# Optimization experiments

Measured on AMD Instinct MI355X. Metric: run time of the kernel, lower is better.

The kernel has to match this reference:

```python
import jax, jax.numpy as jnp
import numpy as np

EXPERT_NUM = 16
TOP_K = 2
BALANCE_WT = 0.01
EPS = 1e-9


def setup_inputs() -> dict:
    key = jax.random.key(0)
    ks = jax.random.split(key, 4)
    B, D, E, O = 8192, 4096, EXPERT_NUM, 512
    features = jax.random.normal(ks[0], (B, D), dtype=jnp.float32)
    W_r = jax.random.normal(ks[1], (D, E), dtype=jnp.float32) * (1.0 / np.sqrt(D))
    b_r = jnp.zeros((E,), dtype=jnp.float32)
    W_e = jax.random.normal(ks[2], (E, D, O), dtype=jnp.float32) * (1.0 / np.sqrt(D))
    b_e = jnp.zeros((E, O), dtype=jnp.float32)
    return {"features": features, "W_r": W_r, "b_r": b_r, "W_e": W_e, "b_e": b_e}


def reference(features, W_r, b_r, W_e, b_e):
    # Router: softmax over experts. [B, E]
    routing_prob = jax.nn.softmax(features @ W_r + b_r, axis=-1)
    # Top-k selection and renormalized combine weights. [B, K]
    top_values, top_indices = jax.lax.top_k(routing_prob, TOP_K)
    weights = top_values / jnp.clip(top_values.sum(axis=1, keepdims=True), EPS)
    # Dense all-expert compute (as the original does). [B, E, O]
    expert_outputs = jnp.einsum('bd,edo->beo', features, W_e) + b_e
    # Gather top-k expert outputs. [B, K, O]
    gathered = jnp.take_along_axis(expert_outputs, top_indices[:, :, None], axis=1)
    logits = jnp.sum(weights[:, :, None] * gathered, axis=1)  # [B, O]
    # Load-balance loss: KL(pi || uniform) scaled by balance_wt.
    pi = routing_prob.mean(axis=0)
    balance_loss = BALANCE_WT * (
        jnp.sum(pi * jnp.log(jnp.clip(pi, EPS)))
        + jnp.log(jnp.asarray(EXPERT_NUM, dtype=pi.dtype))
    )
    return logits, balance_loss
```

## Files before the change

### kernel.cpp

```cpp
#include <hip/hip_runtime.h>


#define B_ 8192
#define D_ 4096
#define E_ 16
#define O_ 512

typedef unsigned int uint32;
typedef unsigned short ushort_t;
typedef __bf16 bf16_t;
typedef bf16_t bf16x8 __attribute__((ext_vector_type(8)));
typedef float f32x4 __attribute__((ext_vector_type(4)));
typedef ushort_t u16x8 __attribute__((ext_vector_type(8)));

__device__ __forceinline__ uint32 bf16_rne(float x) {
  uint32 u = __float_as_uint(x);
  return (u + 0x7fffu + ((u >> 16) & 1u)) >> 16;
}
__device__ __forceinline__ float bf16_to_f32(ushort_t u) {
  return __uint_as_float(((uint32)u) << 16);
}
__device__ __forceinline__ f32x4 ntload4(const float* p) {
  return __builtin_nontemporal_load((const f32x4*)p);
}

__device__ __forceinline__ void gload16(const void* g, void* l) {
  __builtin_amdgcn_global_load_lds(
      (const __attribute__((address_space(1))) void*)g,
      (__attribute__((address_space(3))) void*)l, 16, 0, 0);
}

__global__ __launch_bounds__(256) void wr_transpose(
    const float* __restrict__ Wr, float* __restrict__ WrT) {
  const int d = blockIdx.x * 256 + threadIdx.x;
  const float* src = &Wr[(size_t)d * 16];
  f32x4 v0 = ntload4(src), v1 = ntload4(src + 4);
  f32x4 v2 = ntload4(src + 8), v3 = ntload4(src + 12);
  WrT[0 * D_ + d] = v0[0];  WrT[1 * D_ + d] = v0[1];
  WrT[2 * D_ + d] = v0[2];  WrT[3 * D_ + d] = v0[3];
  WrT[4 * D_ + d] = v1[0];  WrT[5 * D_ + d] = v1[1];
  WrT[6 * D_ + d] = v1[2];  WrT[7 * D_ + d] = v1[3];
  WrT[8 * D_ + d] = v2[0];  WrT[9 * D_ + d] = v2[1];
  WrT[10 * D_ + d] = v2[2]; WrT[11 * D_ + d] = v2[3];
  WrT[12 * D_ + d] = v3[0]; WrT[13 * D_ + d] = v3[1];
  WrT[14 * D_ + d] = v3[2]; WrT[15 * D_ + d] = v3[3];
}

__global__ __launch_bounds__(256) void prep(
    const float* __restrict__ feat, const float* __restrict__ WrT,
    const float* __restrict__ br, const float* __restrict__ We,
    ushort_t* __restrict__ featbf, ushort_t* __restrict__ Wbt,
    int* __restrict__ idxP, float2* __restrict__ wP,
    float* __restrict__ pblk) {
  __shared__ __align__(16) float shmem[64 * 65];
  const int tid = threadIdx.x;

  if (blockIdx.x < 512) {
    const int lane = tid & 63, w = tid >> 6;
    const int tbase = blockIdx.x * 16 + w * 4;

    float acc[4][16] = {};

    for (int si = 0; si < 8; ++si) {
      const int d8 = si * 512 + lane * 8;
      f32x4 fa[4], fb[4];
#pragma unroll
      for (int i = 0; i < 4; ++i) {
        const float* fp = &feat[(size_t)(tbase + i) * D_ + d8];
        fa[i] = ntload4(fp);
        fb[i] = ntload4(fp + 4);
      }
#pragma unroll
      for (int i = 0; i < 4; ++i) {
        uint4 pk;
        pk.x = bf16_rne(fa[i][0]) | (bf16_rne(fa[i][1]) << 16);
        pk.y = bf16_rne(fa[i][2]) | (bf16_rne(fa[i][3]) << 16);
        pk.z = bf16_rne(fb[i][0]) | (bf16_rne(fb[i][1]) << 16);
        pk.w = bf16_rne(fb[i][2]) | (bf16_rne(fb[i][3]) << 16);
        *(uint4*)&featbf[(size_t)(tbase + i) * D_ + d8] = pk;
      }
#pragma unroll
      for (int e = 0; e < 16; ++e) {
        const float* wp = &WrT[(size_t)e * D_ + d8];
        f32x4 wa = *(const f32x4*)wp;
        f32x4 wb = *(const f32x4*)(wp + 4);
#pragma unroll
        for (int i = 0; i < 4; ++i) {
          float a = acc[i][e];
          a = fmaf(fa[i][0], wa[0], a);
          a = fmaf(fa[i][1], wa[1], a);
          a = fmaf(fa[i][2], wa[2], a);
          a = fmaf(fa[i][3], wa[3], a);
          a = fmaf(fb[i][0], wb[0], a);
          a = fmaf(fb[i][1], wb[1], a);
          a = fmaf(fb[i][2], wb[2], a);
          a = fmaf(fb[i][3], wb[3], a);
          acc[i][e] = a;
        }
      }
    }

    float psum[16];
#pragma unroll
    for (int e = 0; e < 16; ++e) psum[e] = 0.f;

#pragma unroll
    for (int i = 0; i < 4; ++i) {
      float l[16];
#pragma unroll
      for (int e = 0; e < 16; ++e) {
        float v = acc[i][e];
#pragma unroll
        for (int m = 32; m >= 1; m >>= 1) v += __shfl_xor(v, m, 64);
        l[e] = v + br[e];
      }
      float mx = l[0];
#pragma unroll
      for (int e = 1; e < 16; ++e) mx = fmaxf(mx, l[e]);
      float p[16];
      float s = 0.f;
#pragma unroll
      for (int e = 0; e < 16; ++e) { p[e] = expf(l[e] - mx); s += p[e]; }
      float inv = 1.f / s;
#pragma unroll
      for (int e = 0; e < 16; ++e) { p[e] *= inv; psum[e] += p[e]; }
      int i0 = 0; float v0 = p[0];
#pragma unroll
      for (int e = 1; e < 16; ++e) if (p[e] > v0) { v0 = p[e]; i0 = e; }
      int i1 = (i0 == 0) ? 1 : 0; float v1 = p[i1];
#pragma unroll
      for (int e = 0; e < 16; ++e)
        if (e != i0 && p[e] > v1) { v1 = p[e]; i1 = e; }
      float denom = fmaxf(v0 + v1, 1e-9f);
      if (lane == 0) {
        int t = tbase + i;
        idxP[t] = i0 | (i1 << 8);
        wP[t] = make_float2(v0 / denom, v1 / denom);
      }
    }
    if (lane == 0) {
#pragma unroll
      for (int e = 0; e < 16; ++e) shmem[w * 16 + e] = psum[e];
    }
    __syncthreads();
    if (tid < 16)
      pblk[blockIdx.x * 16 + tid] =
          (shmem[tid] + shmem[16 + tid]) + (shmem[32 + tid] + shmem[48 + tid]);
  } else {
    const int tx = tid & 15, ty = tid >> 4;
    const int wid = blockIdx.x - 512;
    f32x4 cur[4], nxt[4];
    {
      const int tix = wid * 4;
      const int e = tix >> 9;
      const int rem = tix & 511;
      const int d0 = (rem >> 3) << 6, o0 = (rem & 7) << 6;
      const float* src = We + ((size_t)e * D_ + d0) * O_ + o0;
#pragma unroll
      for (int p = 0; p < 4; ++p)
        cur[p] = ntload4(src + (size_t)(ty + p * 16) * O_ + tx * 4);
    }
#pragma unroll
    for (int q = 0; q < 4; ++q) {
      const int tix = wid * 4 + q;
      const int e = tix >> 9;
      const int rem = tix & 511;
      const int d0 = (rem >> 3) << 6, o0 = (rem & 7) << 6;
      if (q) __syncthreads();
#pragma unroll
      for (int p = 0; p < 4; ++p) {
        int dl = ty + p * 16;
        shmem[dl * 65 + tx * 4 + 0] = cur[p][0];
        shmem[dl * 65 + tx * 4 + 1] = cur[p][1];
        shmem[dl * 65 + tx * 4 + 2] = cur[p][2];
        shmem[dl * 65 + tx * 4 + 3] = cur[p][3];
      }
      if (q < 3) {
        const int tix2 = tix + 1;
        const int e2 = tix2 >> 9;
        const int rem2 = tix2 & 511;
        const int d02 = (rem2 >> 3) << 6, o02 = (rem2 & 7) << 6;
        const float* src2 = We + ((size_t)e2 * D_ + d02) * O_ + o02;
#pragma unroll
        for (int p = 0; p < 4; ++p)
          nxt[p] = ntload4(src2 + (size_t)(ty + p * 16) * O_ + tx * 4);
      }
      __syncthreads();
      ushort_t* dst = Wbt + ((size_t)e * O_ + o0) * D_ + d0;
#pragma unroll
      for (int p = 0; p < 4; ++p) {
        int ol = ty + p * 16;
        uint2 pk;
        pk.x = bf16_rne(shmem[(tx * 4 + 0) * 65 + ol]) |
               (bf16_rne(shmem[(tx * 4 + 1) * 65 + ol]) << 16);
        pk.y = bf16_rne(shmem[(tx * 4 + 2) * 65 + ol]) |
               (bf16_rne(shmem[(tx * 4 + 3) * 65 + ol]) << 16);
        *(uint2*)(dst + (size_t)ol * D_ + tx * 4) = pk;
      }
#pragma unroll
      for (int p = 0; p < 4; ++p) cur[p] = nxt[p];
    }
  }
}

__global__ __launch_bounds__(256) void bucket(
    const int* __restrict__ idxP, const float2* __restrict__ wP,
    int* __restrict__ tokL, float* __restrict__ wgtL, int* __restrict__ cntA,
    int* __restrict__ posA, int* __restrict__ posB) {
  const int e = blockIdx.x;
  const int tid = threadIdx.x, lane = tid & 63, w = tid >> 6;
  __shared__ int wsum[4];
  __shared__ int basev;
  if (tid == 0) basev = 0;
  __syncthreads();

  for (int c = 0; c < B_; c += 256) {
    const int t = c + tid;
    const int pk = idxP[t];
    const float2 wv = wP[t];
    const bool m0 = (pk & 255) == e;
    const bool m1 = (pk >> 8) == e;
    const bool m = m0 || m1;
    const float wt = m0 ? wv.x : wv.y;
    unsigned long long bal = __ballot(m);
    int rank = __popcll(bal & ((1ull << lane) - 1ull));
    if (lane == 0) wsum[w] = __popcll(bal);
    __syncthreads();
    int wbase = basev;
    for (int q = 0; q < w; ++q) wbase += wsum[q];
    if (m) {
      int pos = wbase + rank;
      tokL[e * B_ + pos] = t;
      wgtL[e * B_ + pos] = wt;
      if (m0) posA[t] = pos; else posB[t] = pos;
    }
    __syncthreads();
    if (tid == 0) basev += (wsum[0] + wsum[1]) + (wsum[2] + wsum[3]);
  }
  __syncthreads();
  if (tid == 0) cntA[e] = basev;
}

#define VM3 asm volatile("s_waitcnt vmcnt(3)" ::: "memory")
#define VM0 asm volatile("s_waitcnt vmcnt(0)" ::: "memory")

__global__ __launch_bounds__(512, 4) void moe_gemm(
    const ushort_t* __restrict__ featbf, const ushort_t* __restrict__ Wbt,
    const float* __restrict__ be, const int* __restrict__ tokL,
    const float* __restrict__ wgtL, const int* __restrict__ cntA,
    ushort_t* __restrict__ g0, ushort_t* __restrict__ g1,
    float* __restrict__ out, int dense) {
  const int orig = blockIdx.x;
  const int work = (orig & 7) * 512 + (orig >> 3);
  const int z = work >> 7;
  const int e = z >> 1, khalf = z & 1;
  const int cnt = cntA[e];
  const int row0 = ((work >> 1) & 63) * 128;
  if (row0 >= cnt) return;
  const int o0 = (work & 1) * 256;

  const int tid = threadIdx.x;
  const int lane = tid & 63, w = tid >> 6;
  const int wm = w >> 2, wn = w & 3;

  __shared__ __align__(16) ushort_t As[3][128 * 32];
  __shared__ __align__(16) ushort_t Bs[3][256 * 32];

  const int kg = (lane & 3) ^ ((lane >> 3) & 3);
  const size_t kbase = (size_t)khalf * 2048 + kg * 8;
  const int arow = row0 + w * 16 + (lane >> 2);
  const int atok = (arow < cnt) ? tokL[e * B_ + arow] : 0;
  const ushort_t* aS = featbf + (size_t)atok * D_ + kbase;
  const ushort_t* bS[2];
#pragma unroll
  for (int j = 0; j < 2; ++j) {
    int r = (2 * w + j) * 16 + (lane >> 2);
    bS[j] = Wbt + ((size_t)e * O_ + o0 + r) * D_ + kbase;
  }

  f32x4 acc[4][4] = {};
  const int lr = lane & 15;
  const int lg = lane >> 4;
  const int ps = (lg ^ ((lr >> 1) & 3)) * 8;

#define STAGE(buf, t)                                                \
  {                                                                  \
    gload16(aS + (t) * 32, &As[buf][(w * 16) * 32]);                 \
    gload16(bS[0] + (t) * 32, &Bs[buf][(2 * w) * 512]);              \
    gload16(bS[1] + (t) * 32, &Bs[buf][(2 * w + 1) * 512]);          \
  }

#define COMPUTE(buf)                                                 \
  {                                                                  \
    bf16x8 af[4], bf[4];                                             \
    _Pragma("unroll") for (int m = 0; m < 4; ++m)                    \
        af[m] = *(const bf16x8*)&As[buf][(wm * 64 + m * 16 + lr) * 32 + ps]; \
    _Pragma("unroll") for (int n = 0; n < 4; ++n)                    \
        bf[n] = *(const bf16x8*)&Bs[buf][(wn * 64 + n * 16 + lr) * 32 + ps]; \
    __builtin_amdgcn_s_setprio(1);                                   \
    _Pragma("unroll") for (int m = 0; m < 4; ++m)                    \
        _Pragma("unroll") for (int n = 0; n < 4; ++n)                \
            acc[m][n] = __builtin_amdgcn_mfma_f32_16x16x32_bf16(     \
                af[m], bf[n], acc[m][n], 0, 0, 0);                   \
    __builtin_amdgcn_s_setprio(0);                                   \
  }

  STAGE(0, 0);
  STAGE(1, 1);
  for (int tt = 0; tt < 20; ++tt) {
    const int t = tt * 3;
    VM3; __builtin_amdgcn_s_barrier(); COMPUTE(0); STAGE(2, t + 2);
    VM3; __builtin_amdgcn_s_barrier(); COMPUTE(1); STAGE(0, t + 3);
    VM3; __builtin_amdgcn_s_barrier(); COMPUTE(2); STAGE(1, t + 4);
  }
  VM3; __builtin_amdgcn_s_barrier(); COMPUTE(0); STAGE(2, 62);
  VM3; __builtin_amdgcn_s_barrier(); COMPUTE(1); STAGE(0, 63);
  VM3; __builtin_amdgcn_s_barrier(); COMPUTE(2);
  VM0; __builtin_amdgcn_s_barrier(); COMPUTE(0);

  if (dense) {
    int base = 0;
#pragma unroll
    for (int j = 0; j < 16; ++j) base += (j < e) ? cntA[j] : 0;
    ushort_t* G = khalf ? g1 : g0;
#pragma unroll
    for (int m = 0; m < 4; ++m) {
#pragma unroll
      for (int i = 0; i < 4; ++i) {
        int gr = row0 + wm * 64 + m * 16 + (lane >> 4) * 4 + i;
        if (gr < cnt) {
#pragma unroll
          for (int n = 0; n < 4; ++n) {
            int o = o0 + wn * 64 + n * 16 + (lane & 15);
            G[(size_t)(base + gr) * O_ + o] = (ushort_t)bf16_rne(acc[m][n][i]);
          }
        }
      }
    }
  } else {
#pragma unroll
    for (int m = 0; m < 4; ++m) {
#pragma unroll
      for (int i = 0; i < 4; ++i) {
        int gr = row0 + wm * 64 + m * 16 + (lane >> 4) * 4 + i;
        if (gr < cnt) {
          int tk = tokL[e * B_ + gr];
          float wt = wgtL[e * B_ + gr];
#pragma unroll
          for (int n = 0; n < 4; ++n) {
            int o = o0 + wn * 64 + n * 16 + (lane & 15);
            float v = acc[m][n][i] + (khalf ? 0.f : be[e * O_ + o]);
            atomicAdd(&out[(size_t)tk * O_ + o], wt * v);
          }
        }
      }
    }
  }
#undef STAGE
#undef COMPUTE
}

__global__ __launch_bounds__(256) void combine(
    const ushort_t* __restrict__ g0, const ushort_t* __restrict__ g1,
    const int* __restrict__ idxP, const float2* __restrict__ wP,
    const int* __restrict__ posA, const int* __restrict__ posB,
    const int* __restrict__ cntA, const float* __restrict__ be,
    const float* __restrict__ pblk, float* __restrict__ out) {
  const int tid = threadIdx.x;
  const int t = blockIdx.x * 4 + (tid >> 6);
  const int o = (tid & 63) * 8;
  const int pk = idxP[t];
  const int e0 = pk & 255, e1 = pk >> 8;
  const float2 wv = wP[t];
  int s = 0, off0 = 0, off1 = 0;
#pragma unroll
  for (int j = 0; j < 16; ++j) {
    if (j == e0) off0 = s;
    if (j == e1) off1 = s;
    s += cntA[j];
  }
  const size_t s0 = (size_t)(off0 + posA[t]) * O_ + o;
  const size_t s1 = (size_t)(off1 + posB[t]) * O_ + o;
  u16x8 a0 = *(const u16x8*)&g0[s0];
  u16x8 a1 = *(const u16x8*)&g1[s0];
  u16x8 b0 = *(const u16x8*)&g0[s1];
  u16x8 b1 = *(const u16x8*)&g1[s1];
  const float* be0 = &be[e0 * O_ + o];
  const float* be1 = &be[e1 * O_ + o];
  float r[8];
#pragma unroll
  for (int j = 0; j < 8; ++j) {
    float a = bf16_to_f32(a0[j]) + bf16_to_f32(a1[j]) + be0[j];
    float b = bf16_to_f32(b0[j]) + bf16_to_f32(b1[j]) + be1[j];
    r[j] = wv.x * a + wv.y * b;
  }
  *(f32x4*)&out[(size_t)t * O_ + o] = f32x4{r[0], r[1], r[2], r[3]};
  *(f32x4*)&out[(size_t)t * O_ + o + 4] = f32x4{r[4], r[5], r[6], r[7]};

  if (blockIdx.x == 0) {
    __shared__ float red[64];
    if (tid < 64) {
      const int e = tid & 15, g = tid >> 4;
      float acc = 0.f;
      for (int b = g; b < 512; b += 4) acc += pblk[b * 16 + e];
      red[tid] = acc;
    }
    __syncthreads();
    if (tid < 16) {
      float tot = (red[tid] + red[16 + tid]) + (red[32 + tid] + red[48 + tid]);
      float pi = tot * (1.f / (float)B_);
      red[tid] = pi * logf(fmaxf(pi, 1e-9f));
    }
    __syncthreads();
    if (tid == 0) {
      float loss = 0.f;
#pragma unroll
      for (int e2 = 0; e2 < 16; ++e2) loss += red[e2];
      out[(size_t)B_ * O_] = 0.01f * (loss + logf(16.f));
    }
  }
}

__global__ __launch_bounds__(64) void finalize(const float* __restrict__ pblk,
                                               float* __restrict__ out) {
  __shared__ float red[64];
  const int tid = threadIdx.x;
  const int e = tid & 15, g = tid >> 4;
  float s = 0.f;
  for (int b = g; b < 512; b += 4) s += pblk[b * 16 + e];
  red[tid] = s;
  __syncthreads();
  if (tid < 16) {
    float tot = (red[tid] + red[16 + tid]) + (red[32 + tid] + red[48 + tid]);
    float pi = tot * (1.f / (float)B_);
    red[tid] = pi * logf(fmaxf(pi, 1e-9f));
  }
  __syncthreads();
  if (tid == 0) {
    float loss = 0.f;
#pragma unroll
    for (int e2 = 0; e2 < 16; ++e2) loss += red[e2];
    out[(size_t)B_ * O_] = 0.01f * (loss + logf(16.f));
  }
}

extern "C" void kernel_launch(void* const* d_in, const int* in_sizes, int n_in,
                              void* d_out, int out_size, void* d_ws,
                              size_t ws_size, hipStream_t stream) {
  const float* feat = (const float*)d_in[0];
  const float* Wr = (const float*)d_in[1];
  const float* br = (const float*)d_in[2];
  const float* We = (const float*)d_in[3];
  const float* be = (const float*)d_in[4];
  float* out = (float*)d_out;

  char* ws = (char*)d_ws;
  const size_t SZG     = (size_t)(2 * B_) * O_ * 2;
  const size_t OFF_FEAT = 67108864;
  const size_t OFF_G0   = OFF_FEAT + 67108864;
  const size_t OFF_G1   = OFF_G0 + SZG;
  const size_t OFF_TOK  = OFF_G1 + SZG;
  const size_t OFF_WGT  = OFF_TOK + 524288;
  const size_t OFF_CNT  = OFF_WGT + 524288;
  const size_t OFF_IDX  = OFF_CNT + 256;
  const size_t OFF_WP   = OFF_IDX + 32768;
  const size_t OFF_PB   = OFF_WP + 65536;
  const size_t OFF_PA   = OFF_PB + 32768;
  const size_t OFF_PBo  = OFF_PA + 32768;
  const size_t OFF_WRT  = OFF_PBo + 32768;
  const size_t NEED     = OFF_WRT + 262144;
  ushort_t* Wbt = (ushort_t*)ws;
  ushort_t* featbf = (ushort_t*)(ws + OFF_FEAT);
  ushort_t* g0 = (ushort_t*)(ws + OFF_G0);
  ushort_t* g1 = (ushort_t*)(ws + OFF_G1);
  int* tokL = (int*)(ws + OFF_TOK);
  float* wgtL = (float*)(ws + OFF_WGT);
  int* cntA = (int*)(ws + OFF_CNT);
  int* idxP = (int*)(ws + OFF_IDX);
  float2* wP = (float2*)(ws + OFF_WP);
  float* pblk = (float*)(ws + OFF_PB);
  int* posA = (int*)(ws + OFF_PA);
  int* posB = (int*)(ws + OFF_PBo);
  float* WrT = (float*)(ws + OFF_WRT);
  const int dense = ws_size >= NEED ? 1 : 0;

  if (!dense)
    hipMemsetAsync(out, 0, (size_t)(B_ * O_ + 1) * sizeof(float), stream);

  wr_transpose<<<D_ / 256, 256, 0, stream>>>(Wr, WrT);
  prep<<<512 + 2048, 256, 0, stream>>>(feat, WrT, br, We, featbf, Wbt, idxP,
                                       wP, pblk);
  bucket<<<E_, 256, 0, stream>>>(idxP, wP, tokL, wgtL, cntA, posA, posB);
  moe_gemm<<<4096, 512, 0, stream>>>(featbf, Wbt, be, tokL, wgtL, cntA, g0,
                                     g1, out, dense);
  if (dense)
    combine<<<B_ / 4, 256, 0, stream>>>(g0, g1, idxP, wP, posA, posB, cntA,
                                        be, pblk, out);
  else
    finalize<<<1, 64, 0, stream>>>(pblk, out);
}
```

Measured before the change: 258.5 us.

## Scatter expert GEMM outputs to token-indexed rows and halve router tokens per block

The expert GEMM epilogue now writes each result row straight to a token-indexed slot (first or second choice, chosen through idxP), replacing the compacted per-expert layout. This removes the posA/posB bookkeeping in bucket, the prefix-sum over counts in both the GEMM and combine, and makes combine's reads contiguous by token. Separately, the router part of prep now handles 2 tokens per wave across 1024 blocks instead of 4 tokens across 512, giving more parallelism but loading the router weights more times. The scattered GEMM stores lose some locality, and each stored row needs an extra tokL/idxP lookup.

```diff
diff --git a/kernel.cpp b/kernel.cpp
--- a/kernel.cpp
+++ b/kernel.cpp
@@ -55,23 +55,23 @@
   __shared__ __align__(16) float shmem[64 * 65];
   const int tid = threadIdx.x;
 
-  if (blockIdx.x < 512) {
+  if (blockIdx.x < 1024) {
     const int lane = tid & 63, w = tid >> 6;
-    const int tbase = blockIdx.x * 16 + w * 4;
-
-    float acc[4][16] = {};
+    const int tbase = blockIdx.x * 8 + w * 2;
+
+    float acc[2][16] = {};
 
     for (int si = 0; si < 8; ++si) {
       const int d8 = si * 512 + lane * 8;
-      f32x4 fa[4], fb[4];
-#pragma unroll
-      for (int i = 0; i < 4; ++i) {
+      f32x4 fa[2], fb[2];
+#pragma unroll
+      for (int i = 0; i < 2; ++i) {
         const float* fp = &feat[(size_t)(tbase + i) * D_ + d8];
         fa[i] = ntload4(fp);
         fb[i] = ntload4(fp + 4);
       }
 #pragma unroll
-      for (int i = 0; i < 4; ++i) {
+      for (int i = 0; i < 2; ++i) {
         uint4 pk;
         pk.x = bf16_rne(fa[i][0]) | (bf16_rne(fa[i][1]) << 16);
         pk.y = bf16_rne(fa[i][2]) | (bf16_rne(fa[i][3]) << 16);
@@ -85,7 +85,7 @@
         f32x4 wa = *(const f32x4*)wp;
         f32x4 wb = *(const f32x4*)(wp + 4);
 #pragma unroll
-        for (int i = 0; i < 4; ++i) {
+        for (int i = 0; i < 2; ++i) {
           float a = acc[i][e];
           a = fmaf(fa[i][0], wa[0], a);
           a = fmaf(fa[i][1], wa[1], a);
@@ -105,7 +105,7 @@
     for (int e = 0; e < 16; ++e) psum[e] = 0.f;
 
 #pragma unroll
-    for (int i = 0; i < 4; ++i) {
+    for (int i = 0; i < 2; ++i) {
       float l[16];
 #pragma unroll
       for (int e = 0; e < 16; ++e) {
@@ -148,7 +148,7 @@
           (shmem[tid] + shmem[16 + tid]) + (shmem[32 + tid] + shmem[48 + tid]);
   } else {
     const int tx = tid & 15, ty = tid >> 4;
-    const int wid = blockIdx.x - 512;
+    const int wid = blockIdx.x - 1024;
     f32x4 cur[4], nxt[4];
     {
       const int tix = wid * 4;
@@ -205,8 +205,7 @@
 
 __global__ __launch_bounds__(256) void bucket(
     const int* __restrict__ idxP, const float2* __restrict__ wP,
-    int* __restrict__ tokL, float* __restrict__ wgtL, int* __restrict__ cntA,
-    int* __restrict__ posA, int* __restrict__ posB) {
+    int* __restrict__ tokL, float* __restrict__ wgtL, int* __restrict__ cntA) {
   const int e = blockIdx.x;
   const int tid = threadIdx.x, lane = tid & 63, w = tid >> 6;
   __shared__ int wsum[4];
@@ -232,7 +231,6 @@
       int pos = wbase + rank;
       tokL[e * B_ + pos] = t;
       wgtL[e * B_ + pos] = wt;
-      if (m0) posA[t] = pos; else posB[t] = pos;
     }
     __syncthreads();
     if (tid == 0) basev += (wsum[0] + wsum[1]) + (wsum[2] + wsum[3]);
@@ -248,8 +246,8 @@
     const ushort_t* __restrict__ featbf, const ushort_t* __restrict__ Wbt,
     const float* __restrict__ be, const int* __restrict__ tokL,
     const float* __restrict__ wgtL, const int* __restrict__ cntA,
-    ushort_t* __restrict__ g0, ushort_t* __restrict__ g1,
-    float* __restrict__ out, int dense) {
+    const int* __restrict__ idxP, ushort_t* __restrict__ g0,
+    ushort_t* __restrict__ g1, float* __restrict__ out, int dense) {
   const int orig = blockIdx.x;
   const int work = (orig & 7) * 512 + (orig >> 3);
   const int z = work >> 7;
@@ -319,9 +317,6 @@
   VM0; __builtin_amdgcn_s_barrier(); COMPUTE(0);
 
   if (dense) {
-    int base = 0;
-#pragma unroll
-    for (int j = 0; j < 16; ++j) base += (j < e) ? cntA[j] : 0;
     ushort_t* G = khalf ? g1 : g0;
 #pragma unroll
     for (int m = 0; m < 4; ++m) {
@@ -329,10 +324,12 @@
       for (int i = 0; i < 4; ++i) {
         int gr = row0 + wm * 64 + m * 16 + (lane >> 4) * 4 + i;
         if (gr < cnt) {
+          int tk = tokL[e * B_ + gr];
+          size_t row = ((idxP[tk] & 255) == e) ? (size_t)tk : (size_t)(B_ + tk);
 #pragma unroll
           for (int n = 0; n < 4; ++n) {
             int o = o0 + wn * 64 + n * 16 + (lane & 15);
-            G[(size_t)(base + gr) * O_ + o] = (ushort_t)bf16_rne(acc[m][n][i]);
+            G[row * O_ + o] = (ushort_t)bf16_rne(acc[m][n][i]);
           }
         }
       }
@@ -363,24 +360,16 @@
 __global__ __launch_bounds__(256) void combine(
     const ushort_t* __restrict__ g0, const ushort_t* __restrict__ g1,
     const int* __restrict__ idxP, const float2* __restrict__ wP,
-    const int* __restrict__ posA, const int* __restrict__ posB,
-    const int* __restrict__ cntA, const float* __restrict__ be,
-    const float* __restrict__ pblk, float* __restrict__ out) {
+    const float* __restrict__ be, const float* __restrict__ pblk,
+    float* __restrict__ out) {
   const int tid = threadIdx.x;
   const int t = blockIdx.x * 4 + (tid >> 6);
   const int o = (tid & 63) * 8;
   const int pk = idxP[t];
   const int e0 = pk & 255, e1 = pk >> 8;
   const float2 wv = wP[t];
-  int s = 0, off0 = 0, off1 = 0;
-#pragma unroll
-  for (int j = 0; j < 16; ++j) {
-    if (j == e0) off0 = s;
-    if (j == e1) off1 = s;
-    s += cntA[j];
-  }
-  const size_t s0 = (size_t)(off0 + posA[t]) * O_ + o;
-  const size_t s1 = (size_t)(off1 + posB[t]) * O_ + o;
+  const size_t s0 = (size_t)t * O_ + o;
+  const size_t s1 = (size_t)(B_ + t) * O_ + o;
   u16x8 a0 = *(const u16x8*)&g0[s0];
   u16x8 a1 = *(const u16x8*)&g1[s0];
   u16x8 b0 = *(const u16x8*)&g0[s1];
@@ -402,7 +391,7 @@
     if (tid < 64) {
       const int e = tid & 15, g = tid >> 4;
       float acc = 0.f;
-      for (int b = g; b < 512; b += 4) acc += pblk[b * 16 + e];
+      for (int b = g; b < 1024; b += 4) acc += pblk[b * 16 + e];
       red[tid] = acc;
     }
     __syncthreads();
@@ -427,7 +416,7 @@
   const int tid = threadIdx.x;
   const int e = tid & 15, g = tid >> 4;
   float s = 0.f;
-  for (int b = g; b < 512; b += 4) s += pblk[b * 16 + e];
+  for (int b = g; b < 1024; b += 4) s += pblk[b * 16 + e];
   red[tid] = s;
   __syncthreads();
   if (tid < 16) {
@@ -465,9 +454,7 @@
   const size_t OFF_IDX  = OFF_CNT + 256;
   const size_t OFF_WP   = OFF_IDX + 32768;
   const size_t OFF_PB   = OFF_WP + 65536;
-  const size_t OFF_PA   = OFF_PB + 32768;
-  const size_t OFF_PBo  = OFF_PA + 32768;
-  const size_t OFF_WRT  = OFF_PBo + 32768;
+  const size_t OFF_WRT  = OFF_PB + 65536;
   const size_t NEED     = OFF_WRT + 262144;
   ushort_t* Wbt = (ushort_t*)ws;
   ushort_t* featbf = (ushort_t*)(ws + OFF_FEAT);
@@ -479,8 +466,6 @@
   int* idxP = (int*)(ws + OFF_IDX);
   float2* wP = (float2*)(ws + OFF_WP);
   float* pblk = (float*)(ws + OFF_PB);
-  int* posA = (int*)(ws + OFF_PA);
-  int* posB = (int*)(ws + OFF_PBo);
   float* WrT = (float*)(ws + OFF_WRT);
   const int dense = ws_size >= NEED ? 1 : 0;
 
@@ -488,14 +473,13 @@
     hipMemsetAsync(out, 0, (size_t)(B_ * O_ + 1) * sizeof(float), stream);
 
   wr_transpose<<<D_ / 256, 256, 0, stream>>>(Wr, WrT);
-  prep<<<512 + 2048, 256, 0, stream>>>(feat, WrT, br, We, featbf, Wbt, idxP,
-                                       wP, pblk);
-  bucket<<<E_, 256, 0, stream>>>(idxP, wP, tokL, wgtL, cntA, posA, posB);
-  moe_gemm<<<4096, 512, 0, stream>>>(featbf, Wbt, be, tokL, wgtL, cntA, g0,
-                                     g1, out, dense);
+  prep<<<1024 + 2048, 256, 0, stream>>>(feat, WrT, br, We, featbf, Wbt, idxP,
+                                        wP, pblk);
+  bucket<<<E_, 256, 0, stream>>>(idxP, wP, tokL, wgtL, cntA);
+  moe_gemm<<<4096, 512, 0, stream>>>(featbf, Wbt, be, tokL, wgtL, cntA, idxP,
+                                     g0, g1, out, dense);
   if (dense)
-    combine<<<B_ / 4, 256, 0, stream>>>(g0, g1, idxP, wP, posA, posB, cntA,
-                                        be, pblk, out);
+    combine<<<B_ / 4, 256, 0, stream>>>(g0, g1, idxP, wP, be, pblk, out);
   else
     finalize<<<1, 64, 0, stream>>>(pblk, out);
 }
```

After: 302.4 us. 1.17x slower.
